# Kernel tuning notes

Measured on AMD Instinct MI355X. Metric: run time of the kernel, lower is better.

The kernel has to match this reference:

```python
import jax, jax.numpy as jnp
import numpy as np

L = 2          # num_layers
H = 1024       # hidden_size
XD = 192       # exogenous feature dim
YD = 64        # out_size == y dim
IN = XD + YD   # lstm input size
B = 256
PRE_LEN = 64
FWD_LEN = 48


def setup_inputs() -> dict:
    key = jax.random.key(0)
    ks = jax.random.split(key, 16)
    s = 0.05  # keep gate pre-activations in a sane range
    inp = {
        "pre_x": jax.random.normal(ks[0], (PRE_LEN, B, XD), jnp.float32),
        "pre_y": jax.random.normal(ks[1], (PRE_LEN, B, YD), jnp.float32),
        "forward_x": jax.random.normal(ks[2], (FWD_LEN, B, XD), jnp.float32),
        # layer 0 LSTM params (torch layout: w_ih (4H, IN), w_hh (4H, H))
        "w_ih_0": jax.random.normal(ks[3], (4 * H, IN), jnp.float32) * s,
        "w_hh_0": jax.random.normal(ks[4], (4 * H, H), jnp.float32) * s,
        "b_ih_0": jax.random.normal(ks[5], (4 * H,), jnp.float32) * s,
        "b_hh_0": jax.random.normal(ks[6], (4 * H,), jnp.float32) * s,
        # layer 1
        "w_ih_1": jax.random.normal(ks[7], (4 * H, H), jnp.float32) * s,
        "w_hh_1": jax.random.normal(ks[8], (4 * H, H), jnp.float32) * s,
        "b_ih_1": jax.random.normal(ks[9], (4 * H,), jnp.float32) * s,
        "b_hh_1": jax.random.normal(ks[10], (4 * H,), jnp.float32) * s,
        # fc: Linear(H,H) -> Tanh -> Linear(H,YD)
        "fc_w1": jax.random.normal(ks[11], (H, H), jnp.float32) * s,
        "fc_b1": jax.random.normal(ks[12], (H,), jnp.float32) * s,
        "fc_w2": jax.random.normal(ks[13], (YD, H), jnp.float32) * s,
        "fc_b2": jax.random.normal(ks[14], (YD,), jnp.float32) * s,
    }
    return inp


def _lstm_cell(x, h, c, w_ih, w_hh, b_ih, b_hh):
    # torch gate order: i, f, g, o
    z = x @ w_ih.T + h @ w_hh.T + (b_ih + b_hh)  # (B, 4H)
    i, f, g, o = jnp.split(z, 4, axis=-1)
    c_new = jax.nn.sigmoid(f) * c + jax.nn.sigmoid(i) * jnp.tanh(g)
    h_new = jax.nn.sigmoid(o) * jnp.tanh(c_new)
    return h_new, c_new


def _stack_step(layers, x_t, hs, cs):
    # layers: list of (w_ih, w_hh, b_ih, b_hh); hs, cs: (L, B, H)
    new_h, new_c = [], []
    inp = x_t
    for l, (w_ih, w_hh, b_ih, b_hh) in enumerate(layers):
        h, c = _lstm_cell(inp, hs[l], cs[l], w_ih, w_hh, b_ih, b_hh)
        new_h.append(h)
        new_c.append(c)
        inp = h
    return jnp.stack(new_h), jnp.stack(new_c), inp  # inp = top-layer output


def reference(pre_x, pre_y, forward_x,
              w_ih_0, w_hh_0, b_ih_0, b_hh_0,
              w_ih_1, w_hh_1, b_ih_1, b_hh_1,
              fc_w1, fc_b1, fc_w2, fc_b2):
    layers = [(w_ih_0, w_hh_0, b_ih_0, b_hh_0),
              (w_ih_1, w_hh_1, b_ih_1, b_hh_1)]

    def fc(x):
        return jnp.tanh(x @ fc_w1.T + fc_b1) @ fc_w2.T + fc_b2

    batch = pre_x.shape[1]
    hs0 = jnp.zeros((L, batch, H), pre_x.dtype)
    cs0 = jnp.zeros((L, batch, H), pre_x.dtype)

    # --- warmup encode over concat(pre_x, pre_y) ---
    xy = jnp.concatenate([pre_x, pre_y], axis=2)  # (PRE_LEN, B, IN)

    def enc_step(carry, x_t):
        hs, cs = carry
        hs, cs, top = _stack_step(layers, x_t, hs, cs)
        return (hs, cs), top

    (hs, cs), enc_outs = jax.lax.scan(enc_step, (hs0, cs0), xy)
    top = enc_outs[-1]          # output[-1] from the encoding pass
    last_y = pre_y[-1]

    def dec_step(carry, fx_t):
        hs, cs, top, last_y = carry
        est = fc(top) + last_y                        # (B, YD)
        x_in = jnp.concatenate([fx_t, est], axis=1)   # (B, IN)
        hs, cs, top = _stack_step(layers, x_in, hs, cs)
        return (hs, cs, top, est), est

    _, est_all = jax.lax.scan(dec_step, (hs, cs, top, last_y), forward_x)
    return est_all  # (FWD_LEN, B, YD)
```

## Files before the change

kernel.cpp:

```cpp
#include <hip/hip_runtime.h>
#include <stdint.h>

typedef unsigned short u16;
typedef __attribute__((ext_vector_type(8))) _Float16 f16x8;
typedef __attribute__((ext_vector_type(4))) float f32x4;

__device__ inline f16x8 ldfrag(const u16* p) { return *(const f16x8*)p; }
__device__ inline u16 f2h(float x) {
    _Float16 h = (_Float16)x;
    union { _Float16 h; u16 u; } v; v.h = h;
    return v.u;
}
__device__ inline float sigmoidf_(float x) { return 1.0f / (1.0f + expf(-x)); }


__global__ __launch_bounds__(256, 1) void lstm_cell_k(
    const u16* __restrict__ AFa, int KBa,
    const u16* __restrict__ BFa,
    const u16* __restrict__ AFh,
    const u16* __restrict__ BFh,
    const float* __restrict__ bsum,
    float* __restrict__ c,
    u16* __restrict__ h_out)
{
    const int tid  = threadIdx.x;
    const int w    = tid >> 6;
    const int lane = tid & 63;
    const int l15  = lane & 15;
    const int quad = lane >> 4;
    const int ct   = blockIdx.x;
    const int mg   = blockIdx.y;

    f32x4 acc[4][4];
    #pragma unroll
    for (int t = 0; t < 4; ++t)
        #pragma unroll
        for (int g = 0; g < 4; ++g) acc[t][g] = (f32x4){0, 0, 0, 0};

    {
        const int q = KBa >> 2;
        #pragma unroll 2
        for (int kb = w * q; kb < w * q + q; ++kb) {
            f16x8 a[4], b[4];
            #pragma unroll
            for (int t = 0; t < 4; ++t)
                a[t] = ldfrag(AFa + (((size_t)(mg * 4 + t) * KBa + kb) * 64 + lane) * 8);
            #pragma unroll
            for (int g = 0; g < 4; ++g)
                b[g] = ldfrag(BFa + (((size_t)(ct * 4 + g) * KBa + kb) * 64 + lane) * 8);
            #pragma unroll
            for (int t = 0; t < 4; ++t)
                #pragma unroll
                for (int g = 0; g < 4; ++g)
                    acc[t][g] = __builtin_amdgcn_mfma_f32_16x16x32_f16(a[t], b[g], acc[t][g], 0, 0, 0);
        }
    }
    {
        #pragma unroll 2
        for (int kb = w * 8; kb < w * 8 + 8; ++kb) {
            f16x8 a[4], b[4];
            #pragma unroll
            for (int t = 0; t < 4; ++t)
                a[t] = ldfrag(AFh + (((size_t)(mg * 4 + t) * 32 + kb) * 64 + lane) * 8);
            #pragma unroll
            for (int g = 0; g < 4; ++g)
                b[g] = ldfrag(BFh + (((size_t)(ct * 4 + g) * 32 + kb) * 64 + lane) * 8);
            #pragma unroll
            for (int t = 0; t < 4; ++t)
                #pragma unroll
                for (int g = 0; g < 4; ++g)
                    acc[t][g] = __builtin_amdgcn_mfma_f32_16x16x32_f16(a[t], b[g], acc[t][g], 0, 0, 0);
        }
    }

    __shared__ f32x4 red[4][16][64];
    #pragma unroll
    for (int t = 0; t < 4; ++t)
        #pragma unroll
        for (int g = 0; g < 4; ++g)
            red[w][t * 4 + g][lane] = acc[t][g];
    __syncthreads();

    f32x4 z[4];
    #pragma unroll
    for (int g = 0; g < 4; ++g)
        z[g] = red[0][w * 4 + g][lane] + red[1][w * 4 + g][lane] +
               red[2][w * 4 + g][lane] + red[3][w * 4 + g][lane];

    const int col   = ct * 16 + l15;
    const int mtile = mg * 4 + w;
    float bv[4];
    #pragma unroll
    for (int g = 0; g < 4; ++g) bv[g] = bsum[g * 1024 + col];
    const int hkb = col >> 5, hquad = (col >> 3) & 3, hj = col & 7;
    #pragma unroll
    for (int r = 0; r < 4; ++r) {
        const int rl  = quad * 4 + r;
        const int row = mtile * 16 + rl;
        const size_t gi = (size_t)row * 1024 + col;
        const float zi = z[0][r] + bv[0];
        const float zf = z[1][r] + bv[1];
        const float zg = z[2][r] + bv[2];
        const float zo = z[3][r] + bv[3];
        const float cv = c[gi];
        const float cn = sigmoidf_(zf) * cv + sigmoidf_(zi) * tanhf(zg);
        c[gi] = cn;
        h_out[(((size_t)mtile * 32 + hkb) * 64 + hquad * 16 + rl) * 8 + hj] =
            f2h(sigmoidf_(zo) * tanhf(cn));
    }
}

__global__ __launch_bounds__(256, 1) void fc1_k(
    const u16* __restrict__ AFx,
    const u16* __restrict__ BFw,
    const float* __restrict__ bias,
    u16* __restrict__ U)
{
    const int tid  = threadIdx.x;
    const int w    = tid >> 6;
    const int lane = tid & 63;
    const int l15  = lane & 15;
    const int quad = lane >> 4;
    const int ctq  = blockIdx.x;
    const int mg   = blockIdx.y;

    f32x4 acc[4][4];
    #pragma unroll
    for (int t = 0; t < 4; ++t)
        #pragma unroll
        for (int g = 0; g < 4; ++g) acc[t][g] = (f32x4){0, 0, 0, 0};

    #pragma unroll 2
    for (int kb = w * 8; kb < w * 8 + 8; ++kb) {
        f16x8 a[4], b[4];
        #pragma unroll
        for (int t = 0; t < 4; ++t)
            a[t] = ldfrag(AFx + (((size_t)(mg * 4 + t) * 32 + kb) * 64 + lane) * 8);
        #pragma unroll
        for (int g = 0; g < 4; ++g)
            b[g] = ldfrag(BFw + (((size_t)(ctq * 4 + g) * 32 + kb) * 64 + lane) * 8);
        #pragma unroll
        for (int t = 0; t < 4; ++t)
            #pragma unroll
            for (int g = 0; g < 4; ++g)
                acc[t][g] = __builtin_amdgcn_mfma_f32_16x16x32_f16(a[t], b[g], acc[t][g], 0, 0, 0);
    }

    __shared__ f32x4 red[4][16][64];
    #pragma unroll
    for (int t = 0; t < 4; ++t)
        #pragma unroll
        for (int g = 0; g < 4; ++g)
            red[w][t * 4 + g][lane] = acc[t][g];
    __syncthreads();

    f32x4 z[4];
    #pragma unroll
    for (int g = 0; g < 4; ++g)
        z[g] = red[0][w * 4 + g][lane] + red[1][w * 4 + g][lane] +
               red[2][w * 4 + g][lane] + red[3][w * 4 + g][lane];

    const int mtile = mg * 4 + w;
    #pragma unroll
    for (int g = 0; g < 4; ++g) {
        const int col = ctq * 64 + g * 16 + l15;
        const float bv = bias[col];
        const int ukb = col >> 5, uquad = (col >> 3) & 3, uj = col & 7;
        #pragma unroll
        for (int r = 0; r < 4; ++r) {
            const int rl = quad * 4 + r;
            U[(((size_t)mtile * 32 + ukb) * 64 + uquad * 16 + rl) * 8 + uj] =
                f2h(tanhf(z[g][r] + bv));
        }
    }
}

__global__ __launch_bounds__(256) void fc2_k(
    const u16* __restrict__ AFu,
    const u16* __restrict__ BFw2,
    const float* __restrict__ b2,
    float* __restrict__ est_prev,
    float* __restrict__ out_t,
    u16* __restrict__ xdec_t)
{
    const int tid  = threadIdx.x;
    const int w    = tid >> 6;
    const int lane = tid & 63;
    const int l15  = lane & 15;
    const int quad = lane >> 4;
    const int mtile = blockIdx.x;

    f32x4 accp[4] = {{0,0,0,0},{0,0,0,0},{0,0,0,0},{0,0,0,0}};
    const u16* ap = AFu + ((size_t)(mtile * 32) * 64 + lane) * 8;
    const u16* bp = BFw2 + ((size_t)(w * 32) * 64 + lane) * 8;
    #pragma unroll 4
    for (int kb = 0; kb < 32; ++kb)
        accp[kb & 3] = __builtin_amdgcn_mfma_f32_16x16x32_f16(
            ldfrag(ap + kb * 512), ldfrag(bp + kb * 512), accp[kb & 3], 0, 0, 0);
    f32x4 acc = accp[0] + accp[1] + accp[2] + accp[3];

    const int col = w * 16 + l15;
    const float bv = b2[col];
    const int cx = 192 + col;
    const int xkb = cx >> 5, xquad = (cx >> 3) & 3, xj = cx & 7;
    #pragma unroll
    for (int r = 0; r < 4; ++r) {
        const int rl = quad * 4 + r;
        const int row = mtile * 16 + rl;
        const float v = acc[r] + bv + est_prev[row * 64 + col];
        est_prev[row * 64 + col] = v;
        out_t[row * 64 + col] = v;
        xdec_t[(((size_t)mtile * 8 + xkb) * 64 + xquad * 16 + rl) * 8 + xj] = f2h(v);
    }
}

__global__ void cvt_bfrag_k(const float* __restrict__ src, u16* __restrict__ dst,
                            int K, int kbshift, int S1, int S2, int total) {
    int i = blockIdx.x * 256 + threadIdx.x;
    if (i >= total) return;
    const int lane = i & 63;
    const int kb   = (i >> 6) & ((1 << kbshift) - 1);
    const int rest = i >> (6 + kbshift);
    const int sub  = rest & 3;
    const int grp  = rest >> 2;
    const int row  = sub * S1 + grp * S2 + (lane & 15);
    const int colK = kb * 32 + (lane >> 4) * 8;
    const float* s = src + (size_t)row * K + colK;
    u16* d = dst + (size_t)i * 8;
    #pragma unroll
    for (int j = 0; j < 8; ++j) d[j] = f2h(s[j]);
}
__global__ void bias_k(const float* __restrict__ a, const float* __restrict__ b,
                       float* __restrict__ d, int n) {
    int i = blockIdx.x * 256 + threadIdx.x;
    if (i < n) d[i] = a[i] + b[i];
}
__global__ void init_k(u16* h0, u16* h1, float* c0, float* c1) {
    int i = blockIdx.x * 256 + threadIdx.x;
    h0[i] = 0; h1[i] = 0; c0[i] = 0.0f; c1[i] = 0.0f;
}
__global__ void estinit_k(const float* __restrict__ pre_y, float* __restrict__ est_prev) {
    int i = blockIdx.x * 256 + threadIdx.x;
    est_prev[i] = pre_y[63 * 16384 + i];
}
__global__ void pack_enc_k(const float* __restrict__ pre_x, const float* __restrict__ pre_y,
                           u16* __restrict__ xy) {
    int i = blockIdx.x * 256 + threadIdx.x;
    const int lane  = i & 63;
    const int kb    = (i >> 6) & 7;
    const int mtile = (i >> 9) & 15;
    const int t     = i >> 13;
    const int row   = mtile * 16 + (lane & 15);
    const int cb    = kb * 32 + (lane >> 4) * 8;
    u16* d = xy + (size_t)i * 8;
    #pragma unroll
    for (int j = 0; j < 8; ++j) {
        const int col = cb + j;
        const float v = (col < 192) ? pre_x[((size_t)t * 256 + row) * 192 + col]
                                    : pre_y[((size_t)t * 256 + row) * 64 + (col - 192)];
        d[j] = f2h(v);
    }
}
__global__ void pack_dec_k(const float* __restrict__ fx, u16* __restrict__ xd,
                           int total_threads) {
    int i = blockIdx.x * 256 + threadIdx.x;
    if (i >= total_threads) return;
    const int lane  = i & 63;
    int rest = i >> 6;
    const int kb    = rest % 6;  rest /= 6;
    const int mtile = rest & 15;
    const int t     = rest >> 4;
    const int row   = mtile * 16 + (lane & 15);
    const int cb    = kb * 32 + (lane >> 4) * 8;
    u16* d = xd + ((((size_t)t * 16 + mtile) * 8 + kb) * 64 + lane) * 8;
    #pragma unroll
    for (int j = 0; j < 8; ++j)
        d[j] = f2h(fx[((size_t)t * 256 + row) * 192 + cb + j]);
}

extern "C" void kernel_launch(void* const* d_in, const int* in_sizes, int n_in,
                              void* d_out, int out_size, void* d_ws, size_t ws_size,
                              hipStream_t stream) {
    const float* pre_x  = (const float*)d_in[0];
    const float* pre_y  = (const float*)d_in[1];
    const float* fx     = (const float*)d_in[2];
    const float* w_ih_0 = (const float*)d_in[3];
    const float* w_hh_0 = (const float*)d_in[4];
    const float* b_ih_0 = (const float*)d_in[5];
    const float* b_hh_0 = (const float*)d_in[6];
    const float* w_ih_1 = (const float*)d_in[7];
    const float* w_hh_1 = (const float*)d_in[8];
    const float* b_ih_1 = (const float*)d_in[9];
    const float* b_hh_1 = (const float*)d_in[10];
    const float* fc_w1  = (const float*)d_in[11];
    const float* fc_b1  = (const float*)d_in[12];
    const float* fc_w2  = (const float*)d_in[13];
    const float* fc_b2  = (const float*)d_in[14];

    size_t off = 0;
    char* wsb = (char*)d_ws;
    auto alloc = [&](size_t bytes) -> void* {
        void* p = wsb + off;
        off += (bytes + 255) & ~(size_t)255;
        return p;
    };
    u16* wih0 = (u16*)alloc((size_t)4096 * 256 * 2);
    u16* whh0 = (u16*)alloc((size_t)4096 * 1024 * 2);
    u16* wih1 = (u16*)alloc((size_t)4096 * 1024 * 2);
    u16* whh1 = (u16*)alloc((size_t)4096 * 1024 * 2);
    u16* fcw1 = (u16*)alloc((size_t)1024 * 1024 * 2);
    u16* fcw2 = (u16*)alloc((size_t)64 * 1024 * 2);
    float* b0s = (float*)alloc(4096 * 4);
    float* b1s = (float*)alloc(4096 * 4);
    u16* xyenc = (u16*)alloc((size_t)64 * 256 * 256 * 2);
    u16* xdec  = (u16*)alloc((size_t)48 * 256 * 256 * 2);
    u16* h0b[2] = { (u16*)alloc((size_t)256 * 1024 * 2), (u16*)alloc((size_t)256 * 1024 * 2) };
    u16* h1b[2] = { (u16*)alloc((size_t)256 * 1024 * 2), (u16*)alloc((size_t)256 * 1024 * 2) };
    float* c0 = (float*)alloc((size_t)256 * 1024 * 4);
    float* c1 = (float*)alloc((size_t)256 * 1024 * 4);
    u16* ufc  = (u16*)alloc((size_t)256 * 1024 * 2);
    float* estp = (float*)alloc((size_t)256 * 64 * 4);

    cvt_bfrag_k<<<512, 256, 0, stream>>>(w_ih_0, wih0, 256, 3, 1024, 16, 64 * 4 * 8 * 64);
    cvt_bfrag_k<<<2048, 256, 0, stream>>>(w_hh_0, whh0, 1024, 5, 1024, 16, 64 * 4 * 32 * 64);
    cvt_bfrag_k<<<2048, 256, 0, stream>>>(w_ih_1, wih1, 1024, 5, 1024, 16, 64 * 4 * 32 * 64);
    cvt_bfrag_k<<<2048, 256, 0, stream>>>(w_hh_1, whh1, 1024, 5, 1024, 16, 64 * 4 * 32 * 64);
    cvt_bfrag_k<<<512, 256, 0, stream>>>(fc_w1, fcw1, 1024, 5, 16, 64, 16 * 4 * 32 * 64);
    cvt_bfrag_k<<<32, 256, 0, stream>>>(fc_w2, fcw2, 1024, 5, 16, 0, 1 * 4 * 32 * 64);
    bias_k<<<16, 256, 0, stream>>>(b_ih_0, b_hh_0, b0s, 4096);
    bias_k<<<16, 256, 0, stream>>>(b_ih_1, b_hh_1, b1s, 4096);
    init_k<<<1024, 256, 0, stream>>>(h0b[0], h1b[0], c0, c1);
    estinit_k<<<64, 256, 0, stream>>>(pre_y, estp);
    pack_enc_k<<<2048, 256, 0, stream>>>(pre_x, pre_y, xyenc);
    pack_dec_k<<<1152, 256, 0, stream>>>(fx, xdec, 48 * 16 * 6 * 64);

    int cur = 0;
    for (int t = 0; t < 64; ++t) {
        lstm_cell_k<<<dim3(64, 4), 256, 0, stream>>>(
            xyenc + (size_t)t * 65536, 8, wih0, h0b[cur], whh0, b0s, c0, h0b[1 - cur]);
        lstm_cell_k<<<dim3(64, 4), 256, 0, stream>>>(
            h0b[1 - cur], 32, wih1, h1b[cur], whh1, b1s, c1, h1b[1 - cur]);
        cur ^= 1;
    }
    float* out = (float*)d_out;
    for (int t = 0; t < 48; ++t) {
        fc1_k<<<dim3(16, 4), 256, 0, stream>>>(h1b[cur], fcw1, fc_b1, ufc);
        fc2_k<<<16, 256, 0, stream>>>(ufc, fcw2, fc_b2, estp,
                                      out + (size_t)t * 16384,
                                      xdec + (size_t)t * 65536);
        lstm_cell_k<<<dim3(64, 4), 256, 0, stream>>>(
            xdec + (size_t)t * 65536, 8, wih0, h0b[cur], whh0, b0s, c0, h0b[1 - cur]);
        lstm_cell_k<<<dim3(64, 4), 256, 0, stream>>>(
            h0b[1 - cur], 32, wih1, h1b[cur], whh1, b1s, c1, h1b[1 - cur]);
        cur ^= 1;
    }
}
```

Baseline: 4.011 ms.

## Fuse recurrence into persistent cooperative kernel with grid sync and layer wavefront

Replaces the per-timestep launches with a single cooperative persistent kernel of 256 blocks that uses grid.sync between phases. In the encoder it runs layer 0 at step t and layer 1 at step t-1 in the same phase, which halves the number of barriers. Shared reduction memory is halved by reducing in two passes, and est is double-buffered so concurrent blocks do not race on it. Grid barriers replace launch overhead and may cost more if they are slow; the encoder blocks now do two units of work serially per phase, and a non-cooperative fallback path is kept.

```diff
diff --git a/kernel.cpp b/kernel.cpp
--- a/kernel.cpp
+++ b/kernel.cpp
@@ -1,5 +1,8 @@
 #include <hip/hip_runtime.h>
+#include <hip/hip_cooperative_groups.h>
 #include <stdint.h>
+
+namespace cg = cooperative_groups;
 
 typedef unsigned short u16;
 typedef __attribute__((ext_vector_type(8))) _Float16 f16x8;
@@ -14,22 +17,22 @@
 __device__ inline float sigmoidf_(float x) { return 1.0f / (1.0f + expf(-x)); }
 
 
-__global__ __launch_bounds__(256, 1) void lstm_cell_k(
+typedef f32x4 RedT[8][64];
+
+__device__ __forceinline__ void lstm_unit(
     const u16* __restrict__ AFa, int KBa,
     const u16* __restrict__ BFa,
     const u16* __restrict__ AFh,
     const u16* __restrict__ BFh,
     const float* __restrict__ bsum,
     float* __restrict__ c,
-    u16* __restrict__ h_out)
+    u16* __restrict__ h_out,
+    int ct, int mg, int tid, RedT* red)
 {
-    const int tid  = threadIdx.x;
     const int w    = tid >> 6;
     const int lane = tid & 63;
     const int l15  = lane & 15;
     const int quad = lane >> 4;
-    const int ct   = blockIdx.x;
-    const int mg   = blockIdx.y;
 
     f32x4 acc[4][4];
     #pragma unroll
@@ -73,19 +76,31 @@
         }
     }
 
-    __shared__ f32x4 red[4][16][64];
-    #pragma unroll
-    for (int t = 0; t < 4; ++t)
+    f32x4 z[4];
+    #pragma unroll
+    for (int t = 0; t < 2; ++t)
         #pragma unroll
         for (int g = 0; g < 4; ++g)
             red[w][t * 4 + g][lane] = acc[t][g];
     __syncthreads();
-
-    f32x4 z[4];
-    #pragma unroll
-    for (int g = 0; g < 4; ++g)
-        z[g] = red[0][w * 4 + g][lane] + red[1][w * 4 + g][lane] +
-               red[2][w * 4 + g][lane] + red[3][w * 4 + g][lane];
+    if (w < 2)
+        #pragma unroll
+        for (int g = 0; g < 4; ++g)
+            z[g] = red[0][w * 4 + g][lane] + red[1][w * 4 + g][lane] +
+                   red[2][w * 4 + g][lane] + red[3][w * 4 + g][lane];
+    __syncthreads();
+    #pragma unroll
+    for (int t = 0; t < 2; ++t)
+        #pragma unroll
+        for (int g = 0; g < 4; ++g)
+            red[w][t * 4 + g][lane] = acc[t + 2][g];
+    __syncthreads();
+    if (w >= 2)
+        #pragma unroll
+        for (int g = 0; g < 4; ++g)
+            z[g] = red[0][(w - 2) * 4 + g][lane] + red[1][(w - 2) * 4 + g][lane] +
+                   red[2][(w - 2) * 4 + g][lane] + red[3][(w - 2) * 4 + g][lane];
+    __syncthreads();
 
     const int col   = ct * 16 + l15;
     const int mtile = mg * 4 + w;
@@ -110,19 +125,15 @@
     }
 }
 
-__global__ __launch_bounds__(256, 1) void fc1_k(
-    const u16* __restrict__ AFx,
-    const u16* __restrict__ BFw,
-    const float* __restrict__ bias,
-    u16* __restrict__ U)
+__device__ __forceinline__ void fc1_unit(
+    const u16* __restrict__ AFx, const u16* __restrict__ BFw,
+    const float* __restrict__ bias, u16* __restrict__ U,
+    int ctq, int mg, int tid, RedT* red)
 {
-    const int tid  = threadIdx.x;
     const int w    = tid >> 6;
     const int lane = tid & 63;
     const int l15  = lane & 15;
     const int quad = lane >> 4;
-    const int ctq  = blockIdx.x;
-    const int mg   = blockIdx.y;
 
     f32x4 acc[4][4];
     #pragma unroll
@@ -146,19 +157,31 @@
                 acc[t][g] = __builtin_amdgcn_mfma_f32_16x16x32_f16(a[t], b[g], acc[t][g], 0, 0, 0);
     }
 
-    __shared__ f32x4 red[4][16][64];
-    #pragma unroll
-    for (int t = 0; t < 4; ++t)
+    f32x4 z[4];
+    #pragma unroll
+    for (int t = 0; t < 2; ++t)
         #pragma unroll
         for (int g = 0; g < 4; ++g)
             red[w][t * 4 + g][lane] = acc[t][g];
     __syncthreads();
-
-    f32x4 z[4];
-    #pragma unroll
-    for (int g = 0; g < 4; ++g)
-        z[g] = red[0][w * 4 + g][lane] + red[1][w * 4 + g][lane] +
-               red[2][w * 4 + g][lane] + red[3][w * 4 + g][lane];
+    if (w < 2)
+        #pragma unroll
+        for (int g = 0; g < 4; ++g)
+            z[g] = red[0][w * 4 + g][lane] + red[1][w * 4 + g][lane] +
+                   red[2][w * 4 + g][lane] + red[3][w * 4 + g][lane];
+    __syncthreads();
+    #pragma unroll
+    for (int t = 0; t < 2; ++t)
+        #pragma unroll
+        for (int g = 0; g < 4; ++g)
+            red[w][t * 4 + g][lane] = acc[t + 2][g];
+    __syncthreads();
+    if (w >= 2)
+        #pragma unroll
+        for (int g = 0; g < 4; ++g)
+            z[g] = red[0][(w - 2) * 4 + g][lane] + red[1][(w - 2) * 4 + g][lane] +
+                   red[2][(w - 2) * 4 + g][lane] + red[3][(w - 2) * 4 + g][lane];
+    __syncthreads();
 
     const int mtile = mg * 4 + w;
     #pragma unroll
@@ -175,20 +198,17 @@
     }
 }
 
-__global__ __launch_bounds__(256) void fc2_k(
-    const u16* __restrict__ AFu,
-    const u16* __restrict__ BFw2,
+__device__ __forceinline__ void fc2_unit(
+    const u16* __restrict__ AFu, const u16* __restrict__ BFw2,
     const float* __restrict__ b2,
-    float* __restrict__ est_prev,
-    float* __restrict__ out_t,
-    u16* __restrict__ xdec_t)
+    const float* __restrict__ est_in, float* __restrict__ est_out,
+    float* __restrict__ out_t, u16* __restrict__ xdec_t,
+    int mtile, int tid)
 {
-    const int tid  = threadIdx.x;
     const int w    = tid >> 6;
     const int lane = tid & 63;
     const int l15  = lane & 15;
     const int quad = lane >> 4;
-    const int mtile = blockIdx.x;
 
     f32x4 accp[4] = {{0,0,0,0},{0,0,0,0},{0,0,0,0},{0,0,0,0}};
     const u16* ap = AFu + ((size_t)(mtile * 32) * 64 + lane) * 8;
@@ -207,11 +227,114 @@
     for (int r = 0; r < 4; ++r) {
         const int rl = quad * 4 + r;
         const int row = mtile * 16 + rl;
-        const float v = acc[r] + bv + est_prev[row * 64 + col];
-        est_prev[row * 64 + col] = v;
+        const float v = acc[r] + bv + est_in[row * 64 + col];
+        est_out[row * 64 + col] = v;
         out_t[row * 64 + col] = v;
         xdec_t[(((size_t)mtile * 8 + xkb) * 64 + xquad * 16 + rl) * 8 + xj] = f2h(v);
     }
+}
+
+struct MegaP {
+    const u16 *xyenc; u16 *xdec;
+    const u16 *wih0, *whh0, *wih1, *whh1, *fcw1, *fcw2;
+    const float *b0s, *b1s, *fcb1, *fcb2;
+    float *c0, *c1, *est0, *est1, *out;
+    u16 *h0a, *h0b, *h1a, *h1b, *U;
+};
+
+__global__ __launch_bounds__(256, 1) void mega_k(MegaP p) {
+    cg::grid_group grid = cg::this_grid();
+    __shared__ f32x4 red[4][8][64];
+    const int b   = blockIdx.x;
+    const int tid = threadIdx.x;
+    const int ct  = b & 63;
+    const int mg  = b >> 6;
+
+    u16* h0buf[2] = { p.h0a, p.h0b };
+    u16* h1buf[2] = { p.h1a, p.h1b };
+    float* estb[2] = { p.est0, p.est1 };
+
+    for (int ph = 0; ph <= 64; ++ph) {
+        if (ph < 64)
+            lstm_unit(p.xyenc + (size_t)ph * 65536, 8, p.wih0,
+                      h0buf[ph & 1], p.whh0, p.b0s, p.c0, h0buf[(ph + 1) & 1],
+                      ct, mg, tid, red);
+        if (ph >= 1) {
+            const int t = ph - 1;
+            lstm_unit(h0buf[(t + 1) & 1], 32, p.wih1,
+                      h1buf[t & 1], p.whh1, p.b1s, p.c1, h1buf[(t + 1) & 1],
+                      ct, mg, tid, red);
+        }
+        grid.sync();
+    }
+
+    int cur = 0;
+    for (int t = 0; t < 48; ++t) {
+        if (b < 64)
+            fc1_unit(h1buf[cur], p.fcw1, p.fcb1, p.U, b & 15, b >> 4, tid, red);
+        grid.sync();
+        if (b < 16)
+            fc2_unit(p.U, p.fcw2, p.fcb2, estb[t & 1], estb[(t + 1) & 1],
+                     p.out + (size_t)t * 16384, p.xdec + (size_t)t * 65536, b, tid);
+        grid.sync();
+        lstm_unit(p.xdec + (size_t)t * 65536, 8, p.wih0,
+                  h0buf[cur], p.whh0, p.b0s, p.c0, h0buf[cur ^ 1],
+                  ct, mg, tid, red);
+        grid.sync();
+        lstm_unit(h0buf[cur ^ 1], 32, p.wih1,
+                  h1buf[cur], p.whh1, p.b1s, p.c1, h1buf[cur ^ 1],
+                  ct, mg, tid, red);
+        grid.sync();
+        cur ^= 1;
+    }
+}
+
+__global__ __launch_bounds__(256, 2) void enc_phase_k(MegaP p, int ph) {
+    __shared__ f32x4 red[4][8][64];
+    const int b   = blockIdx.x;
+    const int tid = threadIdx.x;
+    u16* h0buf[2] = { p.h0a, p.h0b };
+    u16* h1buf[2] = { p.h1a, p.h1b };
+    if (b < 256) {
+        if (ph < 64)
+            lstm_unit(p.xyenc + (size_t)ph * 65536, 8, p.wih0,
+                      h0buf[ph & 1], p.whh0, p.b0s, p.c0, h0buf[(ph + 1) & 1],
+                      b & 63, b >> 6, tid, red);
+    } else {
+        if (ph >= 1) {
+            const int t = ph - 1, bb = b - 256;
+            lstm_unit(h0buf[(t + 1) & 1], 32, p.wih1,
+                      h1buf[t & 1], p.whh1, p.b1s, p.c1, h1buf[(t + 1) & 1],
+                      bb & 63, bb >> 6, tid, red);
+        }
+    }
+}
+__global__ __launch_bounds__(256, 2) void fc1_fb_k(MegaP p, int cur) {
+    __shared__ f32x4 red[4][8][64];
+    u16* h1buf[2] = { p.h1a, p.h1b };
+    fc1_unit(h1buf[cur], p.fcw1, p.fcb1, p.U,
+             blockIdx.x & 15, blockIdx.x >> 4, threadIdx.x, red);
+}
+__global__ __launch_bounds__(256, 2) void fc2_fb_k(MegaP p, int t) {
+    float* estb[2] = { p.est0, p.est1 };
+    fc2_unit(p.U, p.fcw2, p.fcb2, estb[t & 1], estb[(t + 1) & 1],
+             p.out + (size_t)t * 16384, p.xdec + (size_t)t * 65536,
+             blockIdx.x, threadIdx.x);
+}
+__global__ __launch_bounds__(256, 2) void l0_fb_k(MegaP p, int t, int cur) {
+    __shared__ f32x4 red[4][8][64];
+    u16* h0buf[2] = { p.h0a, p.h0b };
+    lstm_unit(p.xdec + (size_t)t * 65536, 8, p.wih0,
+              h0buf[cur], p.whh0, p.b0s, p.c0, h0buf[cur ^ 1],
+              blockIdx.x & 63, blockIdx.x >> 6, threadIdx.x, red);
+}
+__global__ __launch_bounds__(256, 2) void l1_fb_k(MegaP p, int cur) {
+    __shared__ f32x4 red[4][8][64];
+    u16* h0buf[2] = { p.h0a, p.h0b };
+    u16* h1buf[2] = { p.h1a, p.h1b };
+    lstm_unit(h0buf[cur ^ 1], 32, p.wih1,
+              h1buf[cur], p.whh1, p.b1s, p.c1, h1buf[cur ^ 1],
+              blockIdx.x & 63, blockIdx.x >> 6, threadIdx.x, red);
 }
 
 __global__ void cvt_bfrag_k(const float* __restrict__ src, u16* __restrict__ dst,
@@ -314,12 +437,15 @@
     float* b1s = (float*)alloc(4096 * 4);
     u16* xyenc = (u16*)alloc((size_t)64 * 256 * 256 * 2);
     u16* xdec  = (u16*)alloc((size_t)48 * 256 * 256 * 2);
-    u16* h0b[2] = { (u16*)alloc((size_t)256 * 1024 * 2), (u16*)alloc((size_t)256 * 1024 * 2) };
-    u16* h1b[2] = { (u16*)alloc((size_t)256 * 1024 * 2), (u16*)alloc((size_t)256 * 1024 * 2) };
+    u16* h0a = (u16*)alloc((size_t)256 * 1024 * 2);
+    u16* h0b = (u16*)alloc((size_t)256 * 1024 * 2);
+    u16* h1a = (u16*)alloc((size_t)256 * 1024 * 2);
+    u16* h1b = (u16*)alloc((size_t)256 * 1024 * 2);
     float* c0 = (float*)alloc((size_t)256 * 1024 * 4);
     float* c1 = (float*)alloc((size_t)256 * 1024 * 4);
     u16* ufc  = (u16*)alloc((size_t)256 * 1024 * 2);
-    float* estp = (float*)alloc((size_t)256 * 64 * 4);
+    float* est0 = (float*)alloc((size_t)256 * 64 * 4);
+    float* est1 = (float*)alloc((size_t)256 * 64 * 4);
 
     cvt_bfrag_k<<<512, 256, 0, stream>>>(w_ih_0, wih0, 256, 3, 1024, 16, 64 * 4 * 8 * 64);
     cvt_bfrag_k<<<2048, 256, 0, stream>>>(w_hh_0, whh0, 1024, 5, 1024, 16, 64 * 4 * 32 * 64);
@@ -329,29 +455,33 @@
     cvt_bfrag_k<<<32, 256, 0, stream>>>(fc_w2, fcw2, 1024, 5, 16, 0, 1 * 4 * 32 * 64);
     bias_k<<<16, 256, 0, stream>>>(b_ih_0, b_hh_0, b0s, 4096);
     bias_k<<<16, 256, 0, stream>>>(b_ih_1, b_hh_1, b1s, 4096);
-    init_k<<<1024, 256, 0, stream>>>(h0b[0], h1b[0], c0, c1);
-    estinit_k<<<64, 256, 0, stream>>>(pre_y, estp);
+    init_k<<<1024, 256, 0, stream>>>(h0a, h1a, c0, c1);
+    estinit_k<<<64, 256, 0, stream>>>(pre_y, est0);
     pack_enc_k<<<2048, 256, 0, stream>>>(pre_x, pre_y, xyenc);
     pack_dec_k<<<1152, 256, 0, stream>>>(fx, xdec, 48 * 16 * 6 * 64);
 
-    int cur = 0;
-    for (int t = 0; t < 64; ++t) {
-        lstm_cell_k<<<dim3(64, 4), 256, 0, stream>>>(
-            xyenc + (size_t)t * 65536, 8, wih0, h0b[cur], whh0, b0s, c0, h0b[1 - cur]);
-        lstm_cell_k<<<dim3(64, 4), 256, 0, stream>>>(
-            h0b[1 - cur], 32, wih1, h1b[cur], whh1, b1s, c1, h1b[1 - cur]);
-        cur ^= 1;
-    }
-    float* out = (float*)d_out;
-    for (int t = 0; t < 48; ++t) {
-        fc1_k<<<dim3(16, 4), 256, 0, stream>>>(h1b[cur], fcw1, fc_b1, ufc);
-        fc2_k<<<16, 256, 0, stream>>>(ufc, fcw2, fc_b2, estp,
-                                      out + (size_t)t * 16384,
-                                      xdec + (size_t)t * 65536);
-        lstm_cell_k<<<dim3(64, 4), 256, 0, stream>>>(
-            xdec + (size_t)t * 65536, 8, wih0, h0b[cur], whh0, b0s, c0, h0b[1 - cur]);
-        lstm_cell_k<<<dim3(64, 4), 256, 0, stream>>>(
-            h0b[1 - cur], 32, wih1, h1b[cur], whh1, b1s, c1, h1b[1 - cur]);
-        cur ^= 1;
-    }
-}
+    MegaP prm;
+    prm.xyenc = xyenc;  prm.xdec = xdec;
+    prm.wih0 = wih0;  prm.whh0 = whh0;  prm.wih1 = wih1;  prm.whh1 = whh1;
+    prm.fcw1 = fcw1;  prm.fcw2 = fcw2;
+    prm.b0s = b0s;  prm.b1s = b1s;  prm.fcb1 = fc_b1;  prm.fcb2 = fc_b2;
+    prm.c0 = c0;  prm.c1 = c1;  prm.est0 = est0;  prm.est1 = est1;
+    prm.out = (float*)d_out;
+    prm.h0a = h0a;  prm.h0b = h0b;  prm.h1a = h1a;  prm.h1b = h1b;  prm.U = ufc;
+
+    void* kargs[] = { (void*)&prm };
+    hipError_t ce = hipLaunchCooperativeKernel((const void*)mega_k, dim3(256), dim3(256),
+                                               kargs, 0, stream);
+    if (ce != hipSuccess) {
+        for (int ph = 0; ph <= 64; ++ph)
+            enc_phase_k<<<512, 256, 0, stream>>>(prm, ph);
+        int cur = 0;
+        for (int t = 0; t < 48; ++t) {
+            fc1_fb_k<<<64, 256, 0, stream>>>(prm, cur);
+            fc2_fb_k<<<16, 256, 0, stream>>>(prm, t);
+            l0_fb_k<<<256, 256, 0, stream>>>(prm, t, cur);
+            l1_fb_k<<<256, 256, 0, stream>>>(prm, cur);
+            cur ^= 1;
+        }
+    }
+}
```

Measured after the change: 11.11 ms. +177.1%, slower.
